# Kernel optimization log

Measured on AMD Instinct MI355X. Metric: run time of the kernel, lower is better.

Reference implementation:

```python
import jax, jax.numpy as jnp
import numpy as np
import math

B, N, M = 4, 512, 64
F, Q, H, R = 256, 16, 8, 32
D = F // H
ETA = 4.0
EPS = 1e-5
FFN_H = 512

def layer_norm(x, g, b):
    mu = jnp.mean(x, axis=-1, keepdims=True)
    var = jnp.mean((x - mu) ** 2, axis=-1, keepdims=True)
    return (x - mu) * jax.lax.rsqrt(var + EPS) * g + b

def setup_inputs() -> dict:
    key = jax.random.key(0)
    ks = jax.random.split(key, 24)
    def xav(k, shape):
        fan_in, fan_out = shape[1], shape[0]
        std = math.sqrt(2.0 / (fan_in + fan_out))
        return jax.random.normal(k, shape, dtype=jnp.float32) * std
    inp = {
        'a': jax.random.normal(ks[0], (B, N, F), dtype=jnp.float32),
        'charges': jax.random.normal(ks[1], (B, N, Q), dtype=jnp.float32),
        'idx_j': jax.random.randint(ks[2], (B, N, M), 0, N),
        'd_ij': jax.random.uniform(ks[3], (B, N, M), dtype=jnp.float32) * 5.0,
        'mask_ij': jax.random.bernoulli(ks[4], 0.3, (B, N, M)),
        'radial_shifts': jnp.linspace(0.5, 5.0, R, dtype=jnp.float32),
        'Wq': xav(ks[5], (F, F + Q)), 'bq': jnp.zeros((F,), jnp.float32),
        'Wk': xav(ks[6], (F, F + Q)), 'bk': jnp.zeros((F,), jnp.float32),
        'Wv': xav(ks[7], (F, F + Q)), 'bv': jnp.zeros((F,), jnp.float32),
        'Wrb': xav(ks[8], (H, R)), 'brb': jnp.zeros((H,), jnp.float32),
        'Wout': xav(ks[9], (F, 2 * F + R)), 'bout': jnp.zeros((F,), jnp.float32),
        'g1': jnp.ones((F,), jnp.float32), 'b1': jnp.zeros((F,), jnp.float32),
        'g2': jnp.ones((F,), jnp.float32), 'b2': jnp.zeros((F,), jnp.float32),
        'Wf1': xav(ks[10], (FFN_H, F)), 'bf1': jnp.zeros((FFN_H,), jnp.float32),
        'Wf2': xav(ks[11], (F, FFN_H)), 'bf2': jnp.zeros((F,), jnp.float32),
    }
    return inp

def reference(a, charges, idx_j, d_ij, mask_ij, radial_shifts,
              Wq, bq, Wk, bk, Wv, bv, Wrb, brb, Wout, bout,
              g1, b1, g2, b2, Wf1, bf1, Wf2, bf2):
    bidx = jnp.arange(B)[:, None, None]
    a_j = a[bidx, idx_j]          # [B,N,M,F]
    q_j = charges[bidx, idx_j]    # [B,N,M,Q]
    center = jnp.concatenate([a, charges], axis=-1)       # [B,N,F+Q]
    neigh = jnp.concatenate([a_j, q_j], axis=-1)          # [B,N,M,F+Q]
    q = (center @ Wq.T + bq).reshape(B, N, H, D)
    k = (neigh @ Wk.T + bk).reshape(B, N, M, H, D)
    v = (neigh @ Wv.T + bv).reshape(B, N, M, H, D)
    # radial basis: exp(-eta*(d - shift)^2)  -> [B,N,M,R]
    radial = jnp.exp(-ETA * (d_ij[..., None] - radial_shifts) ** 2)
    scores = jnp.einsum('bnhd,bnmhd->bnmh', q, k) / math.sqrt(D)
    scores = scores + radial @ Wrb.T + brb                # [B,N,M,H]
    scores = jnp.swapaxes(scores, -1, -2)                 # [B,N,H,M]
    scores = jnp.where(mask_ij[:, :, None, :], -jnp.inf, scores)
    attn = jax.nn.softmax(scores, axis=-1)
    attn = jnp.nan_to_num(attn, nan=0.0, posinf=0.0, neginf=0.0)
    context = jnp.einsum('bnhm,bnmhd->bnhd', attn, v).reshape(B, N, F)
    radial_context = jnp.einsum('bnhm,bnmg->bnhg', attn, radial).mean(axis=-2)  # [B,N,R]
    update = jnp.concatenate([a, context, radial_context], axis=-1) @ Wout.T + bout
    x = layer_norm(a + update, g1, b1)
    ff = jax.nn.gelu(x @ Wf1.T + bf1, approximate=False) @ Wf2.T + bf2
    return layer_norm(x + ff, g2, b2)
```

## Files before the change

kernel.cpp:

```cpp
#include <hip/hip_runtime.h>
#include <hip/hip_bf16.h>
#include <math.h>

#define Bb 4
#define Nn 512
#define Mm 64
#define Ff 256
#define Qq 16
#define Hh 8
#define Rr 32
#define FFNH 512
#define ROWS (Bb*Nn)
#define KIN (Ff+Qq)
#define KINP 288
#define KOUT (2*Ff+Rr)

typedef short short8 __attribute__((ext_vector_type(8)));
typedef unsigned short ushort8 __attribute__((ext_vector_type(8)));
typedef float f32x4 __attribute__((ext_vector_type(4)));

__device__ inline unsigned short f2b(float f) {
    union { float f; unsigned u; } c; c.f = f;
    unsigned r = c.u + 0x7fffu + ((c.u >> 16) & 1u);
    return (unsigned short)(r >> 16);
}
__device__ inline float b2f(unsigned short u) {
    union { unsigned u; float f; } c; c.u = ((unsigned)u) << 16;
    return c.f;
}

#define OFF_CENTER 0
#define OFF_WQKV   (OFF_CENTER + ROWS*KINP)
#define OFF_WOUT   (OFF_WQKV + 768*KINP)
#define OFF_WF1    (OFF_WOUT + Ff*KOUT)
#define OFF_WF2    (OFF_WF1 + FFNH*Ff)
#define OFF_U      (OFF_WF2 + Ff*FFNH)
#define OFF_XB     (OFF_U + ROWS*KOUT)
#define OFF_FFH    (OFF_XB + ROWS*Ff)
#define OFF_QKVB   (OFF_FFH + ROWS*FFNH)
#define CONV_TOTAL OFF_U
#define CONV_BLK4  (CONV_TOTAL/1024)
#define A2U_BLK4   (ROWS*Ff/1024)
#define MSK_BLK16  (Bb*Nn*Mm/(256*16))

__global__ __launch_bounds__(256) void prep(const float* __restrict__ a,
                                            const float* __restrict__ ch,
                                            const float* __restrict__ Wq,
                                            const float* __restrict__ Wk,
                                            const float* __restrict__ Wv,
                                            const float* __restrict__ Wout,
                                            const float* __restrict__ Wf1,
                                            const float* __restrict__ Wf2,
                                            const unsigned char* __restrict__ mask,
                                            int* __restrict__ flag,
                                            unsigned short* __restrict__ arena) {
    int bid = blockIdx.x, tid = threadIdx.x;
    if (bid < CONV_BLK4) {
        int i = (bid * 256 + tid) * 4;
        float4 v4 = {0.f, 0.f, 0.f, 0.f};
        if (i < OFF_WQKV) {
            int row = i / KINP, c = i - row * KINP;
            if (c < Ff)       v4 = *reinterpret_cast<const float4*>(a  + (size_t)row * Ff + c);
            else if (c < KIN) v4 = *reinterpret_cast<const float4*>(ch + (size_t)row * Qq + (c - Ff));
        } else if (i < OFF_WOUT) {
            int j = i - OFF_WQKV;
            int n = j / KINP, c = j - n * KINP;
            const float* W = n < 256 ? Wq : (n < 512 ? Wk : Wv);
            int nr = n & 255;
            if (c < KIN) v4 = *reinterpret_cast<const float4*>(W + (size_t)nr * KIN + c);
        } else if (i < OFF_WF1) {
            v4 = *reinterpret_cast<const float4*>(Wout + (i - OFF_WOUT));
        } else if (i < OFF_WF2) {
            v4 = *reinterpret_cast<const float4*>(Wf1 + (i - OFF_WF1));
        } else {
            v4 = *reinterpret_cast<const float4*>(Wf2 + (i - OFF_WF2));
        }
        ushort4 u;
        u.x = f2b(v4.x); u.y = f2b(v4.y); u.z = f2b(v4.z); u.w = f2b(v4.w);
        *reinterpret_cast<ushort4*>(arena + i) = u;
    } else if (bid < CONV_BLK4 + A2U_BLK4) {
        int j = ((bid - CONV_BLK4) * 256 + tid) * 4;
        int row = j >> 8, col = j & 255;
        float4 v4 = *reinterpret_cast<const float4*>(a + j);
        ushort4 u;
        u.x = f2b(v4.x); u.y = f2b(v4.y); u.z = f2b(v4.z); u.w = f2b(v4.w);
        *reinterpret_cast<ushort4*>(arena + OFF_U + (size_t)row * KOUT + col) = u;
    } else {
        int i = ((bid - CONV_BLK4 - A2U_BLK4) * 256 + tid) * 4;
        const uint4 v = reinterpret_cast<const uint4*>(mask)[i >> 2];
        unsigned m = (v.x | v.y | v.z | v.w) & 0xFFFFFF00u;
        if (m) *flag = 1;
    }
}

template<int KT, int SPLIT, int MODE>
__global__ __launch_bounds__(256) void gemm_mfma(const unsigned short* __restrict__ Ab, int lda,
                                                 const unsigned short* __restrict__ Wb, int ldw,
                                                 const float* __restrict__ b0,
                                                 const float* __restrict__ b1,
                                                 const float* __restrict__ b2,
                                                 float* __restrict__ C,
                                                 unsigned short* __restrict__ Cb,
                                                 int ldc, size_t pstride) {
    __shared__ unsigned short As[2][64][32];
    __shared__ unsigned short Bs[2][64][32];
    int tid = threadIdx.x;
    int colbase = blockIdx.x * 64;
    int rowbase = blockIdx.y * 64;
    constexpr int TPER = (KT + SPLIT - 1) / SPLIT;
    int t0 = blockIdx.z * TPER;
    int NL = KT - t0; if (NL > TPER) NL = TPER;

    int sr = tid >> 2, sl = tid & 3;
    const unsigned short* Ap = Ab + (size_t)(rowbase + sr) * lda + sl * 8;
    const unsigned short* Wp = Wb + (size_t)(colbase + sr) * ldw + sl * 8;
    int ssw = (sl ^ (sr & 3)) * 8;

    int wave = tid >> 6, lane = tid & 63;
    int wr = (wave >> 1) * 32, wc = (wave & 1) * 32;
    int lrow = lane & 15;
    int kslot = lane >> 4;
    int sp = (kslot ^ (lane & 3)) * 8;

    uint4 av, wv;
    auto prefetch = [&](int t) {
        av = *reinterpret_cast<const uint4*>(Ap + (size_t)t * 32);
        wv = *reinterpret_cast<const uint4*>(Wp + (size_t)t * 32);
    };
    auto writeLDS = [&](int buf) {
        *reinterpret_cast<uint4*>(&As[buf][sr][ssw]) = av;
        *reinterpret_cast<uint4*>(&Bs[buf][sr][ssw]) = wv;
    };

    f32x4 acc[2][2] = {};
    prefetch(t0);
    writeLDS(0);
    __syncthreads();
    for (int tt = 0; tt < NL; ++tt) {
        if (tt + 1 < NL) prefetch(t0 + tt + 1);
        int buf = tt & 1;
        short8 a0 = *reinterpret_cast<const short8*>(&As[buf][wr + lrow][sp]);
        short8 a1 = *reinterpret_cast<const short8*>(&As[buf][wr + 16 + lrow][sp]);
        short8 bv0 = *reinterpret_cast<const short8*>(&Bs[buf][wc + lrow][sp]);
        short8 bv1 = *reinterpret_cast<const short8*>(&Bs[buf][wc + 16 + lrow][sp]);
        acc[0][0] = __builtin_amdgcn_mfma_f32_16x16x32_bf16(a0, bv0, acc[0][0], 0, 0, 0);
        acc[0][1] = __builtin_amdgcn_mfma_f32_16x16x32_bf16(a0, bv1, acc[0][1], 0, 0, 0);
        acc[1][0] = __builtin_amdgcn_mfma_f32_16x16x32_bf16(a1, bv0, acc[1][0], 0, 0, 0);
        acc[1][1] = __builtin_amdgcn_mfma_f32_16x16x32_bf16(a1, bv1, acc[1][1], 0, 0, 0);
        if (tt + 1 < NL) {
            writeLDS((tt + 1) & 1);
            __syncthreads();
        }
    }

    const float* bias = b0;
    if (MODE == 1) {
        int sel = colbase >> 8;
        bias = sel == 0 ? b0 : (sel == 1 ? b1 : b2);
    }
    int colq = (colbase & 255);
    float* Cp = (MODE == 0) ? C + (size_t)blockIdx.z * pstride : C;
    #pragma unroll
    for (int fr = 0; fr < 2; ++fr) {
        #pragma unroll
        for (int fc = 0; fc < 2; ++fc) {
            int coll = wc + fc * 16 + (lane & 15);
            int col = colbase + coll;
            #pragma unroll
            for (int i = 0; i < 4; ++i) {
                int row = rowbase + wr + fr * 16 + (lane >> 4) * 4 + i;
                float v = acc[fr][fc][i];
                if (MODE == 0) {
                    Cp[(size_t)row * ldc + col] = v;
                } else if (MODE == 1) {
                    Cb[(size_t)row * ldc + col] = f2b(v + bias[colq + coll]);
                } else {
                    v += bias[col];
                    v = 0.5f * v * (1.0f + erff(v * 0.70710678118654752f));
                    Cb[(size_t)row * ldc + col] = f2b(v);
                }
            }
        }
    }
}

__global__ __launch_bounds__(256) void attn_kernel(const unsigned short* __restrict__ QKV,
                                                   const int* __restrict__ idx_j,
                                                   const float* __restrict__ d_ij,
                                                   const void* __restrict__ mask,
                                                   const float* __restrict__ shifts,
                                                   const float* __restrict__ Wrb,
                                                   const float* __restrict__ brb,
                                                   const int* __restrict__ flag,
                                                   unsigned short* __restrict__ Ub) {
    __shared__ unsigned short Kt[2][16][280];
    __shared__ float rad[Mm][36];
    __shared__ float att[Hh][Mm];
    __shared__ float attbar[Mm];
    __shared__ int   jl[Mm];
    __shared__ float dv[Mm];
    __shared__ int   maskf[Mm];
    __shared__ float shs[Rr];

    int row = blockIdx.x;
    int b = row >> 9;
    int tid = threadIdx.x;
    bool boolmask = (*flag != 0);

    if (tid < Mm) jl[tid] = idx_j[row * Mm + tid];
    else if (tid < 128) { int m = tid - 64; dv[m] = d_ij[row * Mm + m]; }
    else if (tid < 160) shs[tid - 128] = shifts[tid - 128];
    else if (tid >= 192) {
        int m = tid - 192;
        maskf[m] = boolmask ? (int)((const unsigned char*)mask)[row * Mm + m]
                            : ((const int*)mask)[row * Mm + m];
    }

    int half = tid & 1;
    int p = tid >> 1;
    int hh = p >> 4;
    int ml = p & 15;
    float qf[16];
    {
        const unsigned short* qrow = QKV + (size_t)row * 768 + hh * 32 + half * 16;
        ushort8 q0 = *reinterpret_cast<const ushort8*>(qrow);
        ushort8 q1 = *reinterpret_cast<const ushort8*>(qrow + 8);
        #pragma unroll
        for (int i = 0; i < 8; ++i) { qf[i] = b2f(q0[i]); qf[8 + i] = b2f(q1[i]); }
    }
    float4 wreg[4];
    #pragma unroll
    for (int c = 0; c < 4; ++c)
        wreg[c] = *reinterpret_cast<const float4*>(Wrb + hh * Rr + half * 16 + c * 4);
    float brbh = brb[hh];
    __syncthreads();

    auto stage = [&](int t, int seg, int buf) {
        #pragma unroll
        for (int q = 0; q < 2; ++q) {
            int chunk = q * 256 + tid;
            int r = chunk >> 5, s = chunk & 31;
            int j = jl[t * 16 + r];
            const uint4* src = reinterpret_cast<const uint4*>(QKV + (size_t)(b * Nn + j) * 768 + seg);
            uint4 v = src[s];
            *reinterpret_cast<uint4*>(&Kt[buf][r][s * 8]) = v;
        }
    };

    #pragma unroll
    for (int it = 0; it < 8; ++it) {
        int i = tid + it * 256;
        int m = i >> 5, r = i & 31;
        float t = dv[m] - shs[r];
        rad[m][r] = expf(-4.0f * t * t);
    }
    stage(0, 256, 0);
    __syncthreads();

    for (int t = 0; t < 4; ++t) {
        if (t < 3) stage(t + 1, 256, (t + 1) & 1);
        int buf = t & 1;
        const unsigned short* kr = &Kt[buf][ml][hh * 32 + half * 16];
        ushort8 k0 = *reinterpret_cast<const ushort8*>(kr);
        ushort8 k1 = *reinterpret_cast<const ushort8*>(kr + 8);
        float accK = 0.f;
        #pragma unroll
        for (int i = 0; i < 8; ++i) accK = fmaf(qf[i], b2f(k0[i]), accK);
        #pragma unroll
        for (int i = 0; i < 8; ++i) accK = fmaf(qf[8 + i], b2f(k1[i]), accK);
        float accR = 0.f;
        #pragma unroll
        for (int c = 0; c < 4; ++c) {
            float4 rv = *reinterpret_cast<const float4*>(&rad[t * 16 + ml][half * 16 + c * 4]);
            accR += wreg[c].x * rv.x + wreg[c].y * rv.y + wreg[c].z * rv.z + wreg[c].w * rv.w;
        }
        float tv = accK * 0.17677669529663687f + accR;
        tv += __shfl_xor(tv, 1);
        if (!half) {
            int m = t * 16 + ml;
            att[hh][m] = maskf[m] ? -INFINITY : (tv + brbh);
        }
        __syncthreads();
    }

    {
        int h = tid >> 5, l = tid & 31;
        float s0 = att[h][l], s1 = att[h][l + 32];
        float mx = fmaxf(s0, s1);
        #pragma unroll
        for (int off = 16; off; off >>= 1) mx = fmaxf(mx, __shfl_xor(mx, off, 32));
        float e0 = 0.f, e1 = 0.f;
        if (mx != -INFINITY) {
            e0 = expf(s0 - mx);
            e1 = expf(s1 - mx);
        }
        float sm = e0 + e1;
        #pragma unroll
        for (int off = 16; off; off >>= 1) sm += __shfl_xor(sm, off, 32);
        float inv = sm > 0.f ? 1.f / sm : 0.f;
        att[h][l] = e0 * inv;
        att[h][l + 32] = e1 * inv;
    }
    stage(0, 512, 0);
    __syncthreads();

    float ctx = 0.f;
    int h2 = tid >> 5, d0 = tid & 31;
    for (int t = 0; t < 4; ++t) {
        if (t < 3) stage(t + 1, 512, (t + 1) & 1);
        int buf = t & 1;
        #pragma unroll
        for (int m = 0; m < 16; ++m)
            ctx = fmaf(att[h2][t * 16 + m], b2f(Kt[buf][m][h2 * 32 + d0]), ctx);
        if (t == 0 && tid < Mm) {
            float sv = 0.f;
            #pragma unroll
            for (int h = 0; h < Hh; ++h) sv += att[h][tid];
            attbar[tid] = sv * 0.125f;
        }
        __syncthreads();
    }

    Ub[(size_t)row * KOUT + Ff + tid] = f2b(ctx);

    if (tid < 64) {
        int g = tid >> 1;
        float acc = 0.f;
        #pragma unroll
        for (int i = 0; i < 32; ++i) {
            int m = half * 32 + i;
            acc = fmaf(attbar[m], rad[m][g], acc);
        }
        acc += __shfl_xor(acc, 1);
        if (!half) Ub[(size_t)row * KOUT + 2 * Ff + g] = f2b(acc);
    }
}

template<int S, int WB>
__global__ __launch_bounds__(256) void add_ln_c(const float* __restrict__ x0,
                                                const float* __restrict__ part, size_t pstride,
                                                const float* __restrict__ bias,
                                                const float* __restrict__ g,
                                                const float* __restrict__ be,
                                                float* __restrict__ outp,
                                                unsigned short* __restrict__ xb) {
    int tid = threadIdx.x;
    int wave = tid >> 6, lane = tid & 63;
    int row = blockIdx.x * 4 + wave;
    size_t off = (size_t)row * Ff + lane * 4;
    float4 v = *reinterpret_cast<const float4*>(x0 + off);
    float4 bb = *reinterpret_cast<const float4*>(bias + lane * 4);
    v.x += bb.x; v.y += bb.y; v.z += bb.z; v.w += bb.w;
    #pragma unroll
    for (int s = 0; s < S; ++s) {
        float4 p = *reinterpret_cast<const float4*>(part + (size_t)s * pstride + off);
        v.x += p.x; v.y += p.y; v.z += p.z; v.w += p.w;
    }
    float sm = v.x + v.y + v.z + v.w;
    #pragma unroll
    for (int o = 32; o; o >>= 1) sm += __shfl_xor(sm, o, 64);
    float mu = sm * (1.f / Ff);
    float4 c = {v.x - mu, v.y - mu, v.z - mu, v.w - mu};
    float s2 = c.x * c.x + c.y * c.y + c.z * c.z + c.w * c.w;
    #pragma unroll
    for (int o = 32; o; o >>= 1) s2 += __shfl_xor(s2, o, 64);
    float inv = rsqrtf(s2 * (1.f / Ff) + 1e-5f);
    float4 gg = *reinterpret_cast<const float4*>(g + lane * 4);
    float4 ee = *reinterpret_cast<const float4*>(be + lane * 4);
    float4 r;
    r.x = c.x * inv * gg.x + ee.x;
    r.y = c.y * inv * gg.y + ee.y;
    r.z = c.z * inv * gg.z + ee.z;
    r.w = c.w * inv * gg.w + ee.w;
    *reinterpret_cast<float4*>(outp + off) = r;
    if (WB) {
        ushort4 u;
        u.x = f2b(r.x); u.y = f2b(r.y); u.z = f2b(r.z); u.w = f2b(r.w);
        *reinterpret_cast<ushort4*>(&xb[off]) = u;
    }
}

extern "C" void kernel_launch(void* const* d_in, const int* in_sizes, int n_in,
                              void* d_out, int out_size, void* d_ws, size_t ws_size,
                              hipStream_t stream) {
    const float* a       = (const float*)d_in[0];
    const float* charges = (const float*)d_in[1];
    const int*   idx_j   = (const int*)  d_in[2];
    const float* d_ij    = (const float*)d_in[3];
    const void*  mask    =               d_in[4];
    const float* shifts  = (const float*)d_in[5];
    const float* Wq   = (const float*)d_in[6];  const float* bq   = (const float*)d_in[7];
    const float* Wk   = (const float*)d_in[8];  const float* bk   = (const float*)d_in[9];
    const float* Wv   = (const float*)d_in[10]; const float* bv   = (const float*)d_in[11];
    const float* Wrb  = (const float*)d_in[12]; const float* brb  = (const float*)d_in[13];
    const float* Wout = (const float*)d_in[14]; const float* bout = (const float*)d_in[15];
    const float* g1   = (const float*)d_in[16]; const float* b1   = (const float*)d_in[17];
    const float* g2   = (const float*)d_in[18]; const float* b2   = (const float*)d_in[19];
    const float* Wf1  = (const float*)d_in[20]; const float* bf1  = (const float*)d_in[21];
    const float* Wf2  = (const float*)d_in[22]; const float* bf2  = (const float*)d_in[23];
    float* outp = (float*)d_out;

    float* ws   = (float*)d_ws;
    int*   flag = (int*)d_ws;
    float* part = ws + 1024;
    float* xbuf = part + 1048576;
    unsigned short* arena = (unsigned short*)(xbuf + 524288);
    unsigned short* centerb = arena + OFF_CENTER;
    unsigned short* Wqkvb   = arena + OFF_WQKV;
    unsigned short* Woutb   = arena + OFF_WOUT;
    unsigned short* Wf1b    = arena + OFF_WF1;
    unsigned short* Wf2b    = arena + OFF_WF2;
    unsigned short* Ub      = arena + OFF_U;
    unsigned short* xb      = arena + OFF_XB;
    unsigned short* ffhb    = arena + OFF_FFH;
    unsigned short* QKVB16  = arena + OFF_QKVB;

    hipMemsetAsync(flag, 0, sizeof(int), stream);
    prep<<<CONV_BLK4 + A2U_BLK4 + MSK_BLK16, 256, 0, stream>>>(
        a, charges, Wq, Wk, Wv, Wout, Wf1, Wf2, (const unsigned char*)mask, flag, arena);

    gemm_mfma<9, 1, 1><<<dim3(12, 32, 1), 256, 0, stream>>>(
        centerb, KINP, Wqkvb, KINP, bq, bk, bv, nullptr, QKVB16, 768, 0);

    attn_kernel<<<ROWS, 256, 0, stream>>>(QKVB16, idx_j, d_ij, mask, shifts, Wrb, brb, flag, Ub);

    gemm_mfma<17, 2, 0><<<dim3(4, 32, 2), 256, 0, stream>>>(
        Ub, KOUT, Woutb, KOUT, nullptr, nullptr, nullptr, part, nullptr, Ff, (size_t)ROWS * Ff);
    add_ln_c<2, 1><<<ROWS / 4, 256, 0, stream>>>(a, part, (size_t)ROWS * Ff, bout, g1, b1, xbuf, xb);

    gemm_mfma<8, 1, 2><<<dim3(8, 32, 1), 256, 0, stream>>>(
        xb, Ff, Wf1b, Ff, bf1, nullptr, nullptr, nullptr, ffhb, FFNH, 0);

    gemm_mfma<16, 2, 0><<<dim3(4, 32, 2), 256, 0, stream>>>(
        ffhb, FFNH, Wf2b, FFNH, nullptr, nullptr, nullptr, part, nullptr, Ff, (size_t)ROWS * Ff);
    add_ln_c<2, 0><<<ROWS / 4, 256, 0, stream>>>(xbuf, part, (size_t)ROWS * Ff, bf2, g2, b2, outp, nullptr);
}
```

Baseline: 64.28 us.

## Drop memset and a-to-bf16 prep pass, per-block mask flags, split-K 4

Removes the hipMemsetAsync by having each mask-scan block write its own flag entry, which the attention kernel reduces with a wave vote. The bf16 copy of `a` into the output-projection input buffer moves from the prep kernel into the attention kernel. Both split-K GEMMs (Wout and Wf2) go from 2 to 4 partitions, with the partial buffer doubled and the add+LayerNorm kernels summing four partials. QKV/xb/ffh buffers are aliased to save arena space. The cost is more partial-sum traffic in the LayerNorm kernels, traded for more GEMM parallelism and one fewer launch.

```diff
diff --git a/kernel.cpp b/kernel.cpp
--- a/kernel.cpp
+++ b/kernel.cpp
@@ -35,12 +35,12 @@
 #define OFF_WF1    (OFF_WOUT + Ff*KOUT)
 #define OFF_WF2    (OFF_WF1 + FFNH*Ff)
 #define OFF_U      (OFF_WF2 + Ff*FFNH)
-#define OFF_XB     (OFF_U + ROWS*KOUT)
+#define OFF_QKVB   (OFF_U + ROWS*KOUT)
+#define OFF_XB     OFF_QKVB
 #define OFF_FFH    (OFF_XB + ROWS*Ff)
-#define OFF_QKVB   (OFF_FFH + ROWS*FFNH)
+#define ARENA_END  (OFF_QKVB + ROWS*768)
 #define CONV_TOTAL OFF_U
 #define CONV_BLK4  (CONV_TOTAL/1024)
-#define A2U_BLK4   (ROWS*Ff/1024)
 #define MSK_BLK16  (Bb*Nn*Mm/(256*16))
 
 __global__ __launch_bounds__(256) void prep(const float* __restrict__ a,
@@ -52,7 +52,7 @@
                                             const float* __restrict__ Wf1,
                                             const float* __restrict__ Wf2,
                                             const unsigned char* __restrict__ mask,
-                                            int* __restrict__ flag,
+                                            int* __restrict__ flagArr,
                                             unsigned short* __restrict__ arena) {
     int bid = blockIdx.x, tid = threadIdx.x;
     if (bid < CONV_BLK4) {
@@ -78,18 +78,16 @@
         ushort4 u;
         u.x = f2b(v4.x); u.y = f2b(v4.y); u.z = f2b(v4.z); u.w = f2b(v4.w);
         *reinterpret_cast<ushort4*>(arena + i) = u;
-    } else if (bid < CONV_BLK4 + A2U_BLK4) {
-        int j = ((bid - CONV_BLK4) * 256 + tid) * 4;
-        int row = j >> 8, col = j & 255;
-        float4 v4 = *reinterpret_cast<const float4*>(a + j);
-        ushort4 u;
-        u.x = f2b(v4.x); u.y = f2b(v4.y); u.z = f2b(v4.z); u.w = f2b(v4.w);
-        *reinterpret_cast<ushort4*>(arena + OFF_U + (size_t)row * KOUT + col) = u;
     } else {
-        int i = ((bid - CONV_BLK4 - A2U_BLK4) * 256 + tid) * 4;
-        const uint4 v = reinterpret_cast<const uint4*>(mask)[i >> 2];
+        __shared__ int bf_;
+        if (tid == 0) bf_ = 0;
+        __syncthreads();
+        int idx = (bid - CONV_BLK4) * 256 + tid;
+        uint4 v = reinterpret_cast<const uint4*>(mask)[idx];
         unsigned m = (v.x | v.y | v.z | v.w) & 0xFFFFFF00u;
-        if (m) *flag = 1;
+        if (m) atomicOr(&bf_, 1);
+        __syncthreads();
+        if (tid == 0) flagArr[bid - CONV_BLK4] = bf_;
     }
 }
 
@@ -185,13 +183,14 @@
 }
 
 __global__ __launch_bounds__(256) void attn_kernel(const unsigned short* __restrict__ QKV,
+                                                   const float* __restrict__ a,
                                                    const int* __restrict__ idx_j,
                                                    const float* __restrict__ d_ij,
                                                    const void* __restrict__ mask,
                                                    const float* __restrict__ shifts,
                                                    const float* __restrict__ Wrb,
                                                    const float* __restrict__ brb,
-                                                   const int* __restrict__ flag,
+                                                   const int* __restrict__ flagArr,
                                                    unsigned short* __restrict__ Ub) {
     __shared__ unsigned short Kt[2][16][280];
     __shared__ float rad[Mm][36];
@@ -205,7 +204,7 @@
     int row = blockIdx.x;
     int b = row >> 9;
     int tid = threadIdx.x;
-    bool boolmask = (*flag != 0);
+    bool boolmask = __any(flagArr[tid & 31] != 0);
 
     if (tid < Mm) jl[tid] = idx_j[row * Mm + tid];
     else if (tid < 128) { int m = tid - 64; dv[m] = d_ij[row * Mm + m]; }
@@ -321,6 +320,7 @@
         __syncthreads();
     }
 
+    Ub[(size_t)row * KOUT + tid] = f2b(a[(size_t)row * Ff + tid]);
     Ub[(size_t)row * KOUT + Ff + tid] = f2b(ctx);
 
     if (tid < 64) {
@@ -400,10 +400,10 @@
     const float* Wf2  = (const float*)d_in[22]; const float* bf2  = (const float*)d_in[23];
     float* outp = (float*)d_out;
 
-    float* ws   = (float*)d_ws;
-    int*   flag = (int*)d_ws;
+    float* ws      = (float*)d_ws;
+    int*   flagArr = (int*)d_ws;
     float* part = ws + 1024;
-    float* xbuf = part + 1048576;
+    float* xbuf = part + 2097152;
     unsigned short* arena = (unsigned short*)(xbuf + 524288);
     unsigned short* centerb = arena + OFF_CENTER;
     unsigned short* Wqkvb   = arena + OFF_WQKV;
@@ -411,27 +411,26 @@
     unsigned short* Wf1b    = arena + OFF_WF1;
     unsigned short* Wf2b    = arena + OFF_WF2;
     unsigned short* Ub      = arena + OFF_U;
+    unsigned short* QKVB16  = arena + OFF_QKVB;
     unsigned short* xb      = arena + OFF_XB;
     unsigned short* ffhb    = arena + OFF_FFH;
-    unsigned short* QKVB16  = arena + OFF_QKVB;
-
-    hipMemsetAsync(flag, 0, sizeof(int), stream);
-    prep<<<CONV_BLK4 + A2U_BLK4 + MSK_BLK16, 256, 0, stream>>>(
-        a, charges, Wq, Wk, Wv, Wout, Wf1, Wf2, (const unsigned char*)mask, flag, arena);
+
+    prep<<<CONV_BLK4 + MSK_BLK16, 256, 0, stream>>>(
+        a, charges, Wq, Wk, Wv, Wout, Wf1, Wf2, (const unsigned char*)mask, flagArr, arena);
 
     gemm_mfma<9, 1, 1><<<dim3(12, 32, 1), 256, 0, stream>>>(
         centerb, KINP, Wqkvb, KINP, bq, bk, bv, nullptr, QKVB16, 768, 0);
 
-    attn_kernel<<<ROWS, 256, 0, stream>>>(QKVB16, idx_j, d_ij, mask, shifts, Wrb, brb, flag, Ub);
-
-    gemm_mfma<17, 2, 0><<<dim3(4, 32, 2), 256, 0, stream>>>(
+    attn_kernel<<<ROWS, 256, 0, stream>>>(QKVB16, a, idx_j, d_ij, mask, shifts, Wrb, brb, flagArr, Ub);
+
+    gemm_mfma<17, 4, 0><<<dim3(4, 32, 4), 256, 0, stream>>>(
         Ub, KOUT, Woutb, KOUT, nullptr, nullptr, nullptr, part, nullptr, Ff, (size_t)ROWS * Ff);
-    add_ln_c<2, 1><<<ROWS / 4, 256, 0, stream>>>(a, part, (size_t)ROWS * Ff, bout, g1, b1, xbuf, xb);
+    add_ln_c<4, 1><<<ROWS / 4, 256, 0, stream>>>(a, part, (size_t)ROWS * Ff, bout, g1, b1, xbuf, xb);
 
     gemm_mfma<8, 1, 2><<<dim3(8, 32, 1), 256, 0, stream>>>(
         xb, Ff, Wf1b, Ff, bf1, nullptr, nullptr, nullptr, ffhb, FFNH, 0);
 
-    gemm_mfma<16, 2, 0><<<dim3(4, 32, 2), 256, 0, stream>>>(
+    gemm_mfma<16, 4, 0><<<dim3(4, 32, 4), 256, 0, stream>>>(
         ffhb, FFNH, Wf2b, FFNH, nullptr, nullptr, nullptr, part, nullptr, Ff, (size_t)ROWS * Ff);
-    add_ln_c<2, 0><<<ROWS / 4, 256, 0, stream>>>(xbuf, part, (size_t)ROWS * Ff, bf2, g2, b2, outp, nullptr);
-}
+    add_ln_c<4, 0><<<ROWS / 4, 256, 0, stream>>>(xbuf, part, (size_t)ROWS * Ff, bf2, g2, b2, outp, nullptr);
+}
```

New measurement: 64.49 us. Within noise of the previous version (+0.3%).
